# Kernel optimization log

Measured on AMD Instinct MI355X. Metric: run time of the kernel, lower is better.

Reference implementation:

```python
import jax, jax.numpy as jnp
import numpy as np

D = 128          # latent_dim
N = 40000        # num nodes
B = 8            # num graphs in batch
S = N // B       # nodes per graph
K = 6            # knn
E = 640000       # spatial edges
FF = 256         # ffn hidden


def glorot(key, shape):
    lim = jnp.sqrt(6.0 / (shape[0] + shape[-1]))
    return jax.random.uniform(key, shape, minval=-lim, maxval=lim, dtype=jnp.float32)


def setup_inputs() -> dict:
    key = jax.random.key(0)
    ks = jax.random.split(key, 24)
    inp = {
        "x": jax.random.normal(ks[0], (N, D), dtype=jnp.float32),
        "edge_index": jax.random.randint(ks[1], (2, E), 0, N, dtype=jnp.int64),
        "edge_attr": jax.random.uniform(ks[2], (E, 1), dtype=jnp.float32),
        "batch": jnp.repeat(jnp.arange(B, dtype=jnp.int64), S),
        # spatial GATv2Conv params
        "W_sl": glorot(ks[3], (D, D)), "b_sl": jnp.zeros((D,), jnp.float32),
        "W_sr": glorot(ks[4], (D, D)), "b_sr": jnp.zeros((D,), jnp.float32),
        "att_s": glorot(ks[5], (D,)), "W_se": glorot(ks[6], (1, D)),
        "bias_s": jnp.zeros((D,), jnp.float32),
        # latent GATv2Conv params (no edge features)
        "W_ll": glorot(ks[7], (D, D)), "b_ll": jnp.zeros((D,), jnp.float32),
        "W_lr": glorot(ks[8], (D, D)), "b_lr": jnp.zeros((D,), jnp.float32),
        "att_l": glorot(ks[9], (D,)), "bias_l": jnp.zeros((D,), jnp.float32),
        # concat_skip fusion linear: in = 2*D
        "W_c": glorot(ks[10], (2 * D, D)), "b_c": jnp.zeros((D,), jnp.float32),
        # FFN
        "W_f1": glorot(ks[11], (D, FF)), "b_f1": jnp.zeros((FF,), jnp.float32),
        "W_f2": glorot(ks[12], (FF, D)), "b_f2": jnp.zeros((D,), jnp.float32),
    }
    return inp


def relu6(v):
    return jnp.clip(v, 0.0, 6.0)


def segment_softmax(logits, seg, num_segments):
    m = jax.ops.segment_max(logits, seg, num_segments=num_segments)
    e = jnp.exp(logits - m[seg])
    s = jax.ops.segment_sum(e, seg, num_segments=num_segments)
    return e / s[seg]


def gatv2(x, src, dst, edge_feat, W_l, b_l, W_r, b_r, att, bias):
    """PyG GATv2Conv, heads=1, concat=True, negative_slope=0.2."""
    xl = x @ W_l + b_l            # [N,D] source transform
    xr = x @ W_r + b_r            # [N,D] target transform
    h = xl[src] + xr[dst]         # [E,D]
    if edge_feat is not None:
        h = h + edge_feat         # [E,D] already projected by lin_edge
    h = jax.nn.leaky_relu(h, 0.2)
    alpha = h @ att               # [E]
    alpha = segment_softmax(alpha, dst, N)
    out = jax.ops.segment_sum(xl[src] * alpha[:, None], dst, num_segments=N)
    return out + bias


def knn_edges(x):
    """knn_graph(k=K, loop=False, flow='source_to_target') per graph, plus
    the self loops that latent GATv2Conv adds (add_self_loops=True)."""
    xs = jax.lax.stop_gradient(x).reshape(B, S, D)
    sq = jnp.sum(xs * xs, axis=-1)                       # [B,S]
    d2 = sq[:, :, None] + sq[:, None, :] - 2.0 * jnp.einsum('bid,bjd->bij', xs, xs)
    d2 = jnp.where(jnp.eye(S, dtype=bool)[None], jnp.inf, d2)
    _, idx = jax.lax.top_k(-d2, K)                       # [B,S,K] neighbor ids
    offs = (jnp.arange(B) * S)[:, None, None]
    src = (idx + offs).reshape(-1)                       # neighbors -> sources
    dst = jnp.repeat(jnp.arange(N), K)                   # query nodes -> targets
    loop = jnp.arange(N)
    return jnp.concatenate([src, loop]), jnp.concatenate([dst, loop])


def reference(x, edge_index, edge_attr, batch,
              W_sl, b_sl, W_sr, b_sr, att_s, W_se, bias_s,
              W_ll, b_ll, W_lr, b_lr, att_l, bias_l,
              W_c, b_c, W_f1, b_f1, W_f2, b_f2):
    # spatial channel: GATv2 with scalar edge attr
    e_feat = edge_attr @ W_se                            # lin_edge, [E,D]
    ch_sp = gatv2(x, edge_index[0], edge_index[1], e_feat,
                  W_sl, b_sl, W_sr, b_sr, att_s, bias_s)
    # latent channel: dynamic kNN graph + GATv2
    src_l, dst_l = knn_edges(x)
    ch_lat = gatv2(x, src_l, dst_l, None,
                   W_ll, b_ll, W_lr, b_lr, att_l, bias_l)
    # fusion = concat_skip
    fused = jnp.concatenate([ch_sp, ch_lat], axis=-1) @ W_c + b_c + x
    # FFN block (norms are Identity), residual
    ffn = relu6(fused @ W_f1 + b_f1) @ W_f2 + b_f2
    out = fused + ffn
    # plain_last=False -> final activation relu6
    return relu6(out)
```

## Files before the change

### kernel.cpp

```cpp
#include <hip/hip_runtime.h>
#include <math.h>

constexpr int N  = 40000;
constexpr int D  = 128;
constexpr int E  = 640000;
constexpr int Bg = 8;
constexpr int Sg = 5000;
constexpr int KN = 6;
constexpr int FF = 256;
constexpr int CLEN = 640;
constexpr int NCAND = 48;

typedef short short8 __attribute__((ext_vector_type(8)));
typedef float f32x4  __attribute__((ext_vector_type(4)));

__device__ __forceinline__ unsigned short f2bf(float f)
{
    unsigned int u = __float_as_uint(f);
    return (unsigned short)((u + 0x7fffu + ((u >> 16) & 1u)) >> 16);
}

__global__ __launch_bounds__(256) void w_prep_k(
    const float* __restrict__ W0, const float* __restrict__ W1,
    const float* __restrict__ W2, const float* __restrict__ W3,
    const float* __restrict__ Wc, const float* __restrict__ Wf1,
    const float* __restrict__ Wf2,
    unsigned short* __restrict__ wt4, unsigned short* __restrict__ wtc,
    unsigned short* __restrict__ wtf1, unsigned short* __restrict__ wtf2)
{
    int idx = blockIdx.x * 256 + threadIdx.x;
    if (idx < 65536) {
        int m = idx >> 14, rem = idx & 16383;
        int k = rem & 127, c = rem >> 7;
        const float* Wm = (m == 0) ? W0 : (m == 1) ? W1 : (m == 2) ? W2 : W3;
        wt4[m * 16384 + c * 128 + k] = f2bf(Wm[k * 128 + c]);
    } else if (idx < 98304) {
        int rem = idx - 65536; int k = rem & 255, c = rem >> 8;
        wtc[c * 256 + k] = f2bf(Wc[k * 128 + c]);
    } else if (idx < 131072) {
        int rem = idx - 98304; int k = rem & 127, c = rem >> 7;
        wtf1[c * 128 + k] = f2bf(Wf1[k * 256 + c]);
    } else {
        int rem = idx - 131072; int k = rem & 255, c = rem >> 8;
        wtf2[c * 256 + k] = f2bf(Wf2[k * 128 + c]);
    }
}

__global__ __launch_bounds__(256) void gemm_mfma_k(
    const float* __restrict__ A, int lda,
    const unsigned short* __restrict__ Wt, int Kdim,
    const float* __restrict__ bias,
    const float* __restrict__ res,
    float* __restrict__ out, int ldo, int act)
{
    __shared__ float xs[64][36];
    __shared__ unsigned short ws[128][40];
    int tid = threadIdx.x;
    int w = tid >> 6, lane = tid & 63;
    int lg = lane >> 4, ln = lane & 15;
    int r0 = blockIdx.x * 64;
    int cb = blockIdx.y * 128;

    f32x4 acc[8];
#pragma unroll
    for (int ct = 0; ct < 8; ++ct) acc[ct] = {0.f, 0.f, 0.f, 0.f};

    int srow = tid >> 2, sk8 = (tid & 3) * 8;
    int wcol = tid >> 1, wk = (tid & 1) * 16;

    for (int kt = 0; kt < Kdim; kt += 32) {
        __syncthreads();
        *(float4*)&xs[srow][sk8]     = *(const float4*)&A[(size_t)(r0 + srow) * lda + kt + sk8];
        *(float4*)&xs[srow][sk8 + 4] = *(const float4*)&A[(size_t)(r0 + srow) * lda + kt + sk8 + 4];
        *(short8*)&ws[wcol][wk]     = *(const short8*)&Wt[(size_t)(cb + wcol) * Kdim + kt + wk];
        *(short8*)&ws[wcol][wk + 8] = *(const short8*)&Wt[(size_t)(cb + wcol) * Kdim + kt + wk + 8];
        __syncthreads();

        int arow = w * 16 + ln;
        f32x4 a0 = *(const f32x4*)&xs[arow][lg * 8];
        f32x4 a1 = *(const f32x4*)&xs[arow][lg * 8 + 4];
        float af[8] = {a0[0], a0[1], a0[2], a0[3], a1[0], a1[1], a1[2], a1[3]};
        short8 ah, al;
#pragma unroll
        for (int i = 0; i < 8; ++i) {
            unsigned short h = f2bf(af[i]);
            ah[i] = (short)h;
            float hf = __uint_as_float(((unsigned)h) << 16);
            al[i] = (short)f2bf(af[i] - hf);
        }
#pragma unroll
        for (int ct = 0; ct < 8; ++ct) {
            short8 bw = *(const short8*)&ws[ct * 16 + ln][lg * 8];
            acc[ct] = __builtin_amdgcn_mfma_f32_16x16x32_bf16(ah, bw, acc[ct], 0, 0, 0);
            acc[ct] = __builtin_amdgcn_mfma_f32_16x16x32_bf16(al, bw, acc[ct], 0, 0, 0);
        }
    }

#pragma unroll
    for (int ct = 0; ct < 8; ++ct) {
        int c = cb + ct * 16 + ln;
        float bv = bias[c];
#pragma unroll
        for (int rg = 0; rg < 4; ++rg) {
            int r = r0 + w * 16 + lg * 4 + rg;
            float v = acc[ct][rg] + bv;
            if (res) v += res[(size_t)r * 128 + c];
            if (act) v = fminf(fmaxf(v, 0.f), 6.f);
            out[(size_t)r * ldo + c] = v;
        }
    }
}

__global__ __launch_bounds__(256) void gemm4_mfma_k(
    const float* __restrict__ A, const unsigned short* __restrict__ wt4,
    const float* __restrict__ b0, const float* __restrict__ b1,
    const float* __restrict__ b2, const float* __restrict__ b3,
    float* __restrict__ o0, float* __restrict__ o1,
    float* __restrict__ o2, float* __restrict__ o3)
{
    const unsigned short* Wt = wt4 + blockIdx.y * 16384;
    const float* bias; float* out;
    if (blockIdx.y == 0)      { bias = b0; out = o0; }
    else if (blockIdx.y == 1) { bias = b1; out = o1; }
    else if (blockIdx.y == 2) { bias = b2; out = o2; }
    else                      { bias = b3; out = o3; }

    __shared__ float xs[64][36];
    __shared__ unsigned short ws[128][40];
    int tid = threadIdx.x;
    int w = tid >> 6, lane = tid & 63;
    int lg = lane >> 4, ln = lane & 15;
    int r0 = blockIdx.x * 64;

    f32x4 acc[8];
#pragma unroll
    for (int ct = 0; ct < 8; ++ct) acc[ct] = {0.f, 0.f, 0.f, 0.f};

    int srow = tid >> 2, sk8 = (tid & 3) * 8;
    int wcol = tid >> 1, wk = (tid & 1) * 16;

    for (int kt = 0; kt < 128; kt += 32) {
        __syncthreads();
        *(float4*)&xs[srow][sk8]     = *(const float4*)&A[(size_t)(r0 + srow) * 128 + kt + sk8];
        *(float4*)&xs[srow][sk8 + 4] = *(const float4*)&A[(size_t)(r0 + srow) * 128 + kt + sk8 + 4];
        *(short8*)&ws[wcol][wk]     = *(const short8*)&Wt[(size_t)wcol * 128 + kt + wk];
        *(short8*)&ws[wcol][wk + 8] = *(const short8*)&Wt[(size_t)wcol * 128 + kt + wk + 8];
        __syncthreads();

        int arow = w * 16 + ln;
        f32x4 a0 = *(const f32x4*)&xs[arow][lg * 8];
        f32x4 a1 = *(const f32x4*)&xs[arow][lg * 8 + 4];
        float af[8] = {a0[0], a0[1], a0[2], a0[3], a1[0], a1[1], a1[2], a1[3]};
        short8 ah, al;
#pragma unroll
        for (int i = 0; i < 8; ++i) {
            unsigned short h = f2bf(af[i]);
            ah[i] = (short)h;
            float hf = __uint_as_float(((unsigned)h) << 16);
            al[i] = (short)f2bf(af[i] - hf);
        }
#pragma unroll
        for (int ct = 0; ct < 8; ++ct) {
            short8 bw = *(const short8*)&ws[ct * 16 + ln][lg * 8];
            acc[ct] = __builtin_amdgcn_mfma_f32_16x16x32_bf16(ah, bw, acc[ct], 0, 0, 0);
            acc[ct] = __builtin_amdgcn_mfma_f32_16x16x32_bf16(al, bw, acc[ct], 0, 0, 0);
        }
    }

#pragma unroll
    for (int ct = 0; ct < 8; ++ct) {
        int c = ct * 16 + ln;
        float bv = bias[c];
#pragma unroll
        for (int rg = 0; rg < 4; ++rg) {
            int r = r0 + w * 16 + lg * 4 + rg;
            out[(size_t)r * 128 + c] = acc[ct][rg] + bv;
        }
    }
}

__global__ __launch_bounds__(256) void prep_k(const float* __restrict__ x,
                                              unsigned short* __restrict__ xh,
                                              float* __restrict__ sqn)
{
    int w = threadIdx.x >> 6, lane = threadIdx.x & 63;
    int row = blockIdx.x * 4 + w;
    float2 v = *(const float2*)&x[(size_t)row * 128 + lane * 2];
    ushort2 h = make_ushort2(f2bf(v.x), f2bf(v.y));
    *(ushort2*)&xh[(size_t)row * 128 + lane * 2] = h;
    float s = fmaf(v.y, v.y, v.x * v.x);
#pragma unroll
    for (int off = 32; off; off >>= 1) s += __shfl_xor(s, off);
    if (lane == 0) sqn[row] = s;
}

__device__ __forceinline__ void ins6(unsigned (&d)[6], unsigned k)
{
#pragma unroll
    for (int t = 0; t < 6; ++t) {
        unsigned lo = d[t] < k ? d[t] : k;
        unsigned hi = d[t] < k ? k : d[t];
        d[t] = lo; k = hi;
    }
}

__global__ __launch_bounds__(256) void knn_mfma_k(const unsigned short* __restrict__ xh,
                                                  const float* __restrict__ sqn,
                                                  int* __restrict__ cand)
{
    __shared__ char lds[16640];
    char* ldsH = lds;
    float* cs_s = (float*)(lds + 16384);

    int b = blockIdx.x;
    int g = b & 7, r = b >> 3;
    int chunk = r & 7, qblk = r >> 3;
    int gbase = g * Sg;
    int cbase = chunk * CLEN;
    int qlen = (chunk < 7) ? CLEN : (Sg - 7 * CLEN);
    int ntiles = (qlen + 63) >> 6;
    int nfull = (chunk < 7) ? ntiles : ntiles - 1;
    int tid = threadIdx.x;
    int w = tid >> 6, lane = tid & 63;
    int lg = lane >> 4, ln = lane & 15;
    int q0 = qblk * 128 + w * 32;

    short8 bh[2][4];
#pragma unroll
    for (int s = 0; s < 2; ++s) {
        int q = q0 + s * 16 + ln;
        int qrow = gbase + (q < Sg ? q : Sg - 1);
#pragma unroll
        for (int ks = 0; ks < 4; ++ks)
            bh[s][ks] = *(const short8*)&xh[(size_t)qrow * 128 + ks * 32 + lg * 8];
    }

    int srow = tid >> 4, sslot = tid & 15;
    int sw_st = (srow & 7) << 4;
    int dstoff[4];
    const unsigned short* src[4];
#pragma unroll
    for (int i = 0; i < 4; ++i) {
        int row = i * 16 + srow;
        dstoff[i] = row * 256 + ((sslot * 16) ^ sw_st);
        src[i] = &xh[(size_t)(gbase + cbase + row) * 128 + sslot * 8];
    }
    const float* csrc = &sqn[gbase + cbase];

    unsigned d6a[6], d6b[6];
#pragma unroll
    for (int t = 0; t < 6; ++t) { d6a[t] = 0xFFFFFFFFu; d6b[t] = 0xFFFFFFFFu; }

    for (int t64 = 0; t64 < ntiles; ++t64) {
        __syncthreads();
        if (t64 < nfull) {
#pragma unroll
            for (int i = 0; i < 4; ++i) {
                short8 vh = *(const short8*)src[i];
                src[i] += 64 * 128;
                *(short8*)(ldsH + dstoff[i]) = vh;
            }
            if (tid < 64) cs_s[tid] = csrc[tid] + 1024.0f;
        } else {
            int c0 = cbase + t64 * 64;
#pragma unroll
            for (int i = 0; i < 4; ++i) {
                int cr = c0 + i * 16 + srow;
                if (cr >= Sg) cr = Sg - 1;
                short8 vh = *(const short8*)&xh[(size_t)(gbase + cr) * 128 + sslot * 8];
                *(short8*)(ldsH + dstoff[i]) = vh;
            }
            if (tid < 64) {
                int cl = c0 + tid;
                cs_s[tid] = (cl < cbase + qlen) ? (sqn[gbase + cl] + 1024.0f) : __builtin_inff();
            }
        }
        csrc += 64;
        __syncthreads();

        int c0 = cbase + t64 * 64;
#pragma unroll
        for (int g16 = 0; g16 < 4; ++g16) {
            f32x4 acc0 = {0.f, 0.f, 0.f, 0.f};
            f32x4 acc1 = {0.f, 0.f, 0.f, 0.f};
            int rr = g16 * 16 + ln;
            int rsw = (ln & 7) << 4;
#pragma unroll
            for (int ks = 0; ks < 4; ++ks) {
                short8 ah = *(const short8*)(ldsH + rr * 256 + ((lg * 16 + ks * 64) ^ rsw));
                acc0 = __builtin_amdgcn_mfma_f32_16x16x32_bf16(ah, bh[0][ks], acc0, 0, 0, 0);
                acc1 = __builtin_amdgcn_mfma_f32_16x16x32_bf16(ah, bh[1][ks], acc1, 0, 0, 0);
            }
            f32x4 cv = *(const f32x4*)&cs_s[g16 * 16 + lg * 4];
            int idx0 = (c0 - cbase) + g16 * 16 + lg * 4;
#pragma unroll
            for (int rg = 0; rg < 4; ++rg) {
                unsigned ki = (unsigned)(idx0 + rg);
                unsigned k0 = (__float_as_uint(fmaf(-2.f, acc0[rg], cv[rg])) & 0xFFFFF800u) | ki;
                unsigned k1 = (__float_as_uint(fmaf(-2.f, acc1[rg], cv[rg])) & 0xFFFFF800u) | ki;
                ins6(d6a, k0);
                ins6(d6b, k1);
            }
        }
    }

#pragma unroll
    for (int s = 0; s < 2; ++s) {
        unsigned m6[6];
#pragma unroll
        for (int t = 0; t < 6; ++t) m6[t] = s ? d6b[t] : d6a[t];
#pragma unroll
        for (int sg = 1; sg < 4; ++sg)
#pragma unroll
            for (int t = 0; t < 6; ++t) {
                unsigned v = __shfl(s ? d6b[t] : d6a[t], ln + sg * 16);
#pragma unroll
                for (int u = 0; u < 6; ++u) {
                    unsigned lo = m6[u] < v ? m6[u] : v;
                    unsigned hi = m6[u] < v ? v : m6[u];
                    m6[u] = lo; v = hi;
                }
            }
        int q = q0 + s * 16 + ln;
        if (lg == 0 && q < Sg) {
            int* cp = &cand[(size_t)(gbase + q) * NCAND + chunk * 6];
#pragma unroll
            for (int t = 0; t < 6; ++t) cp[t] = gbase + cbase + (int)(m6[t] & 2047u);
        }
    }
}

__global__ __launch_bounds__(256) void knn_rerank_k(const float* __restrict__ x,
                                                    const float* __restrict__ sqn,
                                                    const int* __restrict__ cand,
                                                    int* __restrict__ knn_idx)
{
    int w = threadIdx.x >> 6, lane = threadIdx.x & 63;
    int grp = lane >> 4, gl = lane & 15;
    int q = blockIdx.x * 4 + w;
    float4 qa = *(const float4*)&x[(size_t)q * 128 + gl * 8];
    float4 qb = *(const float4*)&x[(size_t)q * 128 + gl * 8 + 4];
    const int* cp = &cand[(size_t)q * NCAND + grp * 12];

    int ca[12]; unsigned okm = 0;
#pragma unroll
    for (int j = 0; j < 12; ++j) {
        int c = cp[j];
        bool ok = (unsigned)c < (unsigned)N && c != q;
        okm |= (ok ? 1u : 0u) << j;
        ca[j] = ok ? c : 0;
    }

    float d6[6]; int i6[6]; float mx = __builtin_inff(); int sl = 0;
#pragma unroll
    for (int t = 0; t < 6; ++t) { d6[t] = __builtin_inff(); i6[t] = -1; }

    float4 vaA = *(const float4*)&x[(size_t)ca[0] * 128 + gl * 8];
    float4 vbA = *(const float4*)&x[(size_t)ca[0] * 128 + gl * 8 + 4];
#pragma unroll
    for (int j = 0; j < 12; ++j) {
        float4 vaB, vbB;
        if (j < 11) {
            vaB = *(const float4*)&x[(size_t)ca[j + 1] * 128 + gl * 8];
            vbB = *(const float4*)&x[(size_t)ca[j + 1] * 128 + gl * 8 + 4];
        }
        float p = qa.x * vaA.x;
        p = fmaf(qa.y, vaA.y, p); p = fmaf(qa.z, vaA.z, p); p = fmaf(qa.w, vaA.w, p);
        p = fmaf(qb.x, vbA.x, p); p = fmaf(qb.y, vbA.y, p);
        p = fmaf(qb.z, vbA.z, p); p = fmaf(qb.w, vbA.w, p);
#pragma unroll
        for (int off = 1; off < 16; off <<= 1) p += __shfl_xor(p, off);
        float dv = ((okm >> j) & 1u) ? fmaf(-2.f, p, sqn[ca[j]]) : __builtin_inff();
        if (dv < mx) {
#pragma unroll
            for (int t = 0; t < 6; ++t)
                if (t == sl) { d6[t] = dv; i6[t] = ca[j]; }
            float m2 = d6[0]; int s2 = 0;
#pragma unroll
            for (int t = 1; t < 6; ++t)
                if (d6[t] > m2) { m2 = d6[t]; s2 = t; }
            mx = m2; sl = s2;
        }
        vaA = vaB; vbA = vbB;
    }

#pragma unroll
    for (int sg = 1; sg < 4; ++sg) {
#pragma unroll
        for (int t = 0; t < 6; ++t) {
            float dv = __shfl(d6[t], gl + sg * 16);
            int ci = __shfl(i6[t], gl + sg * 16);
            if (grp == 0 && dv < mx) {
#pragma unroll
                for (int u = 0; u < 6; ++u)
                    if (u == sl) { d6[u] = dv; i6[u] = ci; }
                float m2 = d6[0]; int s2 = 0;
#pragma unroll
                for (int u = 1; u < 6; ++u)
                    if (d6[u] > m2) { m2 = d6[u]; s2 = u; }
                mx = m2; sl = s2;
            }
        }
    }
    if (lane < 6) {
        int v;
#pragma unroll
        for (int t = 0; t < 6; ++t) if (t == lane) v = i6[t];
        knn_idx[(size_t)q * 6 + lane] = v;
    }
}

__global__ __launch_bounds__(256) void hist_k(const int* __restrict__ dstA, int* __restrict__ deg)
{
    int e = blockIdx.x * 256 + threadIdx.x;
    atomicAdd(&deg[dstA[e]], 1);
}

__global__ __launch_bounds__(1024) void scan_k(const int* __restrict__ deg, int* __restrict__ rowptr)
{
    __shared__ int ps[1024];
    int t = threadIdx.x;
    const int chunk = 40;
    int base = t * chunk;
    int s = 0;
    for (int k = 0; k < chunk; ++k) { int i = base + k; if (i < N) s += deg[i]; }
    ps[t] = s;
    __syncthreads();
    for (int off = 1; off < 1024; off <<= 1) {
        int v = (t >= off) ? ps[t - off] : 0;
        __syncthreads();
        ps[t] += v;
        __syncthreads();
    }
    int run = ps[t] - s;
    for (int k = 0; k < chunk; ++k) {
        int i = base + k;
        if (i < N) { rowptr[i] = run; run += deg[i]; }
    }
    if (t == 0) rowptr[N] = E;
}

__global__ __launch_bounds__(256) void scatter_k(const int* __restrict__ srcA, const int* __restrict__ dstA,
                                                 const float* __restrict__ ea,
                                                 const int* __restrict__ rowptr, int* __restrict__ cnt,
                                                 int* __restrict__ csr_src, float* __restrict__ csr_ea)
{
    int e = blockIdx.x * 256 + threadIdx.x;
    int d = dstA[e];
    int pos = rowptr[d] + atomicAdd(&cnt[d], 1);
    csr_src[pos] = srcA[e];
    csr_ea[pos] = ea[e];
}

__global__ __launch_bounds__(256) void gat_fused_k(
    const float* __restrict__ xl_s, const float* __restrict__ xr_s,
    const int* __restrict__ rowptr, const int* __restrict__ csr_src, const float* __restrict__ csr_ea,
    const float* __restrict__ att_s, const float* __restrict__ wse, const float* __restrict__ bias_s,
    const float* __restrict__ xl_l, const float* __restrict__ xr_l,
    const int* __restrict__ knn, const float* __restrict__ att_l, const float* __restrict__ bias_l,
    float* __restrict__ ch2)
{
    int w = threadIdx.x >> 6, lane = threadIdx.x & 63;
    int dst = blockIdx.x * 4 + w;

    if (blockIdx.y == 0) {
        int base = rowptr[dst];
        int deg = rowptr[dst + 1] - base;
        float xr0 = xr_s[(size_t)dst * 128 + lane], xr1 = xr_s[(size_t)dst * 128 + 64 + lane];
        float at0 = att_s[lane], at1 = att_s[64 + lane];
        float we0 = wse[lane], we1 = wse[64 + lane];

        float eaN = 0.f, v0N = 0.f, v1N = 0.f;
        if (deg > 0) {
            int s0 = csr_src[base];
            eaN = csr_ea[base];
            v0N = xl_s[(size_t)s0 * 128 + lane];
            v1N = xl_s[(size_t)s0 * 128 + 64 + lane];
        }
        float m = -1e30f, ssum = 0.f, o0 = 0.f, o1 = 0.f;
        for (int i = 0; i < deg; ++i) {
            float ea = eaN, v0 = v0N, v1 = v1N;
            if (i + 1 < deg) {
                int sn = csr_src[base + i + 1];
                eaN = csr_ea[base + i + 1];
                v0N = xl_s[(size_t)sn * 128 + lane];
                v1N = xl_s[(size_t)sn * 128 + 64 + lane];
            }
            float h0 = fmaf(ea, we0, v0 + xr0);
            float h1 = fmaf(ea, we1, v1 + xr1);
            h0 = h0 > 0.f ? h0 : 0.2f * h0;
            h1 = h1 > 0.f ? h1 : 0.2f * h1;
            float p = fmaf(h1, at1, h0 * at0);
#pragma unroll
            for (int off = 32; off; off >>= 1) p += __shfl_xor(p, off);
            if (p <= m) {
                float wt = __expf(p - m);
                ssum += wt;
                o0 = fmaf(wt, v0, o0);
                o1 = fmaf(wt, v1, o1);
            } else {
                float sc = __expf(m - p);
                ssum = fmaf(ssum, sc, 1.f);
                o0 = fmaf(o0, sc, v0);
                o1 = fmaf(o1, sc, v1);
                m = p;
            }
        }
        float inv = deg > 0 ? 1.f / ssum : 0.f;
        ch2[(size_t)dst * 256 + lane]      = fmaf(o0, inv, bias_s[lane]);
        ch2[(size_t)dst * 256 + 64 + lane] = fmaf(o1, inv, bias_s[64 + lane]);
    } else {
        float xr0 = xr_l[(size_t)dst * 128 + lane], xr1 = xr_l[(size_t)dst * 128 + 64 + lane];
        float at0 = att_l[lane], at1 = att_l[64 + lane];
        int s[7];
#pragma unroll
        for (int j = 0; j < 6; ++j) s[j] = knn[(size_t)dst * 6 + j];
        s[6] = dst;
        float l[7];
#pragma unroll
        for (int j = 0; j < 7; ++j) {
            float h0 = xl_l[(size_t)s[j] * 128 + lane] + xr0;
            float h1 = xl_l[(size_t)s[j] * 128 + 64 + lane] + xr1;
            h0 = h0 > 0.f ? h0 : 0.2f * h0;
            h1 = h1 > 0.f ? h1 : 0.2f * h1;
            float p = h0 * at0 + h1 * at1;
#pragma unroll
            for (int off = 32; off; off >>= 1) p += __shfl_xor(p, off);
            l[j] = p;
        }
        float m = l[0];
#pragma unroll
        for (int j = 1; j < 7; ++j) m = fmaxf(m, l[j]);
        float sum = 0.f;
#pragma unroll
        for (int j = 0; j < 7; ++j) { l[j] = __expf(l[j] - m); sum += l[j]; }
        float inv = 1.f / sum;
        float o0 = 0.f, o1 = 0.f;
#pragma unroll
        for (int j = 0; j < 7; ++j) {
            float a = l[j] * inv;
            o0 = fmaf(a, xl_l[(size_t)s[j] * 128 + lane], o0);
            o1 = fmaf(a, xl_l[(size_t)s[j] * 128 + 64 + lane], o1);
        }
        ch2[(size_t)dst * 256 + 128 + lane] = o0 + bias_l[lane];
        ch2[(size_t)dst * 256 + 192 + lane] = o1 + bias_l[64 + lane];
    }
}

extern "C" void kernel_launch(void* const* d_in, const int* in_sizes, int n_in,
                              void* d_out, int out_size, void* d_ws, size_t ws_size,
                              hipStream_t stream)
{
    const float* x      = (const float*)d_in[0];
    const int*   ei     = (const int*)  d_in[1];
    const float* eattr  = (const float*)d_in[2];
    const float* W_sl   = (const float*)d_in[4];
    const float* b_sl   = (const float*)d_in[5];
    const float* W_sr   = (const float*)d_in[6];
    const float* b_sr   = (const float*)d_in[7];
    const float* att_s  = (const float*)d_in[8];
    const float* W_se   = (const float*)d_in[9];
    const float* bias_s = (const float*)d_in[10];
    const float* W_ll   = (const float*)d_in[11];
    const float* b_ll   = (const float*)d_in[12];
    const float* W_lr   = (const float*)d_in[13];
    const float* b_lr   = (const float*)d_in[14];
    const float* att_l  = (const float*)d_in[15];
    const float* bias_l = (const float*)d_in[16];
    const float* W_c    = (const float*)d_in[17];
    const float* b_c    = (const float*)d_in[18];
    const float* W_f1   = (const float*)d_in[19];
    const float* b_f1   = (const float*)d_in[20];
    const float* W_f2   = (const float*)d_in[21];
    const float* b_f2   = (const float*)d_in[22];
    float* out = (float*)d_out;

    char* wp = (char*)d_ws;
    auto take = [&](size_t bytes) { char* p = wp; wp += (bytes + 255) & ~(size_t)255; return p; };
    float* xl_s    = (float*)take((size_t)N * D * 4);
    float* xr_s    = (float*)take((size_t)N * D * 4);
    float* xl_l    = (float*)take((size_t)N * D * 4);
    float* xr_l    = (float*)take((size_t)N * D * 4);
    float* ch2     = (float*)take((size_t)N * 2 * D * 4);
    float* sqn     = (float*)take((size_t)N * 4);
    int*   knn_idx = (int*)  take((size_t)N * KN * 4);
    int*   deg     = (int*)  take((size_t)N * 4);
    int*   rowptr  = (int*)  take((size_t)(N + 1) * 4);
    int*   csr_src = (int*)  take((size_t)E * 4);
    float* csr_ea  = (float*)take((size_t)E * 4);
    unsigned short* x_hi = (unsigned short*)take((size_t)N * D * 2);
    int*   knn_cand = (int*)take((size_t)N * NCAND * 4);
    unsigned short* wt4  = (unsigned short*)take(65536 * 2);
    unsigned short* wtc  = (unsigned short*)take(32768 * 2);
    unsigned short* wtf1 = (unsigned short*)take(32768 * 2);
    unsigned short* wtf2 = (unsigned short*)take(32768 * 2);
    float* fused   = xl_s;
    float* hbuf    = ch2;
    if ((size_t)(wp - (char*)d_ws) > ws_size) return;

    dim3 blk(256);

    w_prep_k<<<dim3(640), blk, 0, stream>>>(W_sl, W_sr, W_ll, W_lr, W_c, W_f1, W_f2,
                                            wt4, wtc, wtf1, wtf2);

    gemm4_mfma_k<<<dim3(N / 64, 4), blk, 0, stream>>>(x, wt4,
        b_sl, b_sr, b_ll, b_lr, xl_s, xr_s, xl_l, xr_l);

    prep_k<<<dim3(N / 4), blk, 0, stream>>>(x, x_hi, sqn);
    knn_mfma_k<<<dim3(Bg * 40 * 8), blk, 0, stream>>>(x_hi, sqn, knn_cand);
    knn_rerank_k<<<dim3(N / 4), blk, 0, stream>>>(x, sqn, knn_cand, knn_idx);

    hipMemsetAsync(deg, 0, (size_t)N * 4, stream);
    hist_k<<<dim3(E / 256), blk, 0, stream>>>(ei + E, deg);
    scan_k<<<dim3(1), dim3(1024), 0, stream>>>(deg, rowptr);
    hipMemsetAsync(deg, 0, (size_t)N * 4, stream);
    scatter_k<<<dim3(E / 256), blk, 0, stream>>>(ei, ei + E, eattr, rowptr, deg, csr_src, csr_ea);

    gat_fused_k<<<dim3(N / 4, 2), blk, 0, stream>>>(xl_s, xr_s, rowptr, csr_src, csr_ea,
                                                    att_s, W_se, bias_s,
                                                    xl_l, xr_l, knn_idx, att_l, bias_l, ch2);

    gemm_mfma_k<<<dim3(N / 64, 1), blk, 0, stream>>>(ch2, 2 * D, wtc, 256, b_c, x, fused, 128, 0);
    gemm_mfma_k<<<dim3(N / 64, 2), blk, 0, stream>>>(fused, 128, wtf1, 128, b_f1, nullptr, hbuf, 256, 1);
    gemm_mfma_k<<<dim3(N / 64, 1), blk, 0, stream>>>(hbuf, 256, wtf2, 256, b_f2, fused, out, 128, 1);
}
```

Baseline: 521.2 us.

## Fuse bf16 prep into projection GEMM and stage two kNN tiles per sync

The separate prep kernel that converts x to bf16 and computes squared norms is removed. That work now runs inside the y==0 blocks of the four-way projection GEMM, reusing the x tiles those blocks already load, which saves a launch and a full read of x. The kNN kernel doubles its LDS to two tile buffers, stages two candidate tiles between barriers, and splits the MFMA accumulation from the top-6 insertion to halve barrier count. The cost is more LDS per block, which may lower occupancy, and extra work concentrated in the y==0 GEMM blocks.

```diff
diff --git a/kernel.cpp b/kernel.cpp
--- a/kernel.cpp
+++ b/kernel.cpp
@@ -116,7 +116,8 @@
     const float* __restrict__ b0, const float* __restrict__ b1,
     const float* __restrict__ b2, const float* __restrict__ b3,
     float* __restrict__ o0, float* __restrict__ o1,
-    float* __restrict__ o2, float* __restrict__ o3)
+    float* __restrict__ o2, float* __restrict__ o3,
+    unsigned short* __restrict__ xh, float* __restrict__ sqn)
 {
     const unsigned short* Wt = wt4 + blockIdx.y * 16384;
     const float* bias; float* out;
@@ -138,13 +139,27 @@
 
     int srow = tid >> 2, sk8 = (tid & 3) * 8;
     int wcol = tid >> 1, wk = (tid & 1) * 16;
+    bool emit = (blockIdx.y == 0);
+    float sq = 0.f;
 
     for (int kt = 0; kt < 128; kt += 32) {
         __syncthreads();
-        *(float4*)&xs[srow][sk8]     = *(const float4*)&A[(size_t)(r0 + srow) * 128 + kt + sk8];
-        *(float4*)&xs[srow][sk8 + 4] = *(const float4*)&A[(size_t)(r0 + srow) * 128 + kt + sk8 + 4];
+        float4 v0 = *(const float4*)&A[(size_t)(r0 + srow) * 128 + kt + sk8];
+        float4 v1 = *(const float4*)&A[(size_t)(r0 + srow) * 128 + kt + sk8 + 4];
+        *(float4*)&xs[srow][sk8]     = v0;
+        *(float4*)&xs[srow][sk8 + 4] = v1;
         *(short8*)&ws[wcol][wk]     = *(const short8*)&Wt[(size_t)wcol * 128 + kt + wk];
         *(short8*)&ws[wcol][wk + 8] = *(const short8*)&Wt[(size_t)wcol * 128 + kt + wk + 8];
+        if (emit) {
+            float f[8] = {v0.x, v0.y, v0.z, v0.w, v1.x, v1.y, v1.z, v1.w};
+            short8 hv;
+#pragma unroll
+            for (int i = 0; i < 8; ++i) {
+                hv[i] = (short)f2bf(f[i]);
+                sq = fmaf(f[i], f[i], sq);
+            }
+            *(short8*)&xh[(size_t)(r0 + srow) * 128 + kt + sk8] = hv;
+        }
         __syncthreads();
 
         int arow = w * 16 + ln;
@@ -167,6 +182,12 @@
         }
     }
 
+    if (emit) {
+        sq += __shfl_xor(sq, 1);
+        sq += __shfl_xor(sq, 2);
+        if ((tid & 3) == 0) sqn[r0 + srow] = sq;
+    }
+
 #pragma unroll
     for (int ct = 0; ct < 8; ++ct) {
         int c = ct * 16 + ln;
@@ -177,21 +198,6 @@
             out[(size_t)r * 128 + c] = acc[ct][rg] + bv;
         }
     }
-}
-
-__global__ __launch_bounds__(256) void prep_k(const float* __restrict__ x,
-                                              unsigned short* __restrict__ xh,
-                                              float* __restrict__ sqn)
-{
-    int w = threadIdx.x >> 6, lane = threadIdx.x & 63;
-    int row = blockIdx.x * 4 + w;
-    float2 v = *(const float2*)&x[(size_t)row * 128 + lane * 2];
-    ushort2 h = make_ushort2(f2bf(v.x), f2bf(v.y));
-    *(ushort2*)&xh[(size_t)row * 128 + lane * 2] = h;
-    float s = fmaf(v.y, v.y, v.x * v.x);
-#pragma unroll
-    for (int off = 32; off; off >>= 1) s += __shfl_xor(s, off);
-    if (lane == 0) sqn[row] = s;
 }
 
 __device__ __forceinline__ void ins6(unsigned (&d)[6], unsigned k)
@@ -208,9 +214,7 @@
                                                   const float* __restrict__ sqn,
                                                   int* __restrict__ cand)
 {
-    __shared__ char lds[16640];
-    char* ldsH = lds;
-    float* cs_s = (float*)(lds + 16384);
+    __shared__ char lds[33280];
 
     int b = blockIdx.x;
     int g = b & 7, r = b >> 3;
@@ -238,12 +242,12 @@
     int srow = tid >> 4, sslot = tid & 15;
     int sw_st = (srow & 7) << 4;
     int dstoff[4];
-    const unsigned short* src[4];
+    const unsigned short* srcb[4];
 #pragma unroll
     for (int i = 0; i < 4; ++i) {
         int row = i * 16 + srow;
         dstoff[i] = row * 256 + ((sslot * 16) ^ sw_st);
-        src[i] = &xh[(size_t)(gbase + cbase + row) * 128 + sslot * 8];
+        srcb[i] = &xh[(size_t)(gbase + cbase + row) * 128 + sslot * 8];
     }
     const float* csrc = &sqn[gbase + cbase];
 
@@ -251,34 +255,36 @@
 #pragma unroll
     for (int t = 0; t < 6; ++t) { d6a[t] = 0xFFFFFFFFu; d6b[t] = 0xFFFFFFFFu; }
 
-    for (int t64 = 0; t64 < ntiles; ++t64) {
-        __syncthreads();
+    auto stage = [&](int t64, int buf) {
+        char* dst = lds + buf * 16384;
+        float* cs = (float*)(lds + 32768 + buf * 256);
         if (t64 < nfull) {
-#pragma unroll
-            for (int i = 0; i < 4; ++i) {
-                short8 vh = *(const short8*)src[i];
-                src[i] += 64 * 128;
-                *(short8*)(ldsH + dstoff[i]) = vh;
-            }
-            if (tid < 64) cs_s[tid] = csrc[tid] + 1024.0f;
+            size_t off = (size_t)t64 * 64 * 128;
+#pragma unroll
+            for (int i = 0; i < 4; ++i)
+                *(short8*)(dst + dstoff[i]) = *(const short8*)(srcb[i] + off);
+            if (tid < 64) cs[tid] = csrc[t64 * 64 + tid] + 1024.0f;
         } else {
             int c0 = cbase + t64 * 64;
 #pragma unroll
             for (int i = 0; i < 4; ++i) {
                 int cr = c0 + i * 16 + srow;
                 if (cr >= Sg) cr = Sg - 1;
-                short8 vh = *(const short8*)&xh[(size_t)(gbase + cr) * 128 + sslot * 8];
-                *(short8*)(ldsH + dstoff[i]) = vh;
+                *(short8*)(dst + dstoff[i]) =
+                    *(const short8*)&xh[(size_t)(gbase + cr) * 128 + sslot * 8];
             }
             if (tid < 64) {
                 int cl = c0 + tid;
-                cs_s[tid] = (cl < cbase + qlen) ? (sqn[gbase + cl] + 1024.0f) : __builtin_inff();
-            }
-        }
-        csrc += 64;
-        __syncthreads();
-
-        int c0 = cbase + t64 * 64;
+                cs[tid] = (cl < cbase + qlen) ? (sqn[gbase + cl] + 1024.0f) : __builtin_inff();
+            }
+        }
+    };
+
+    auto compute = [&](int t64, int buf) {
+        const char* ldsH = lds + buf * 16384;
+        const float* cs = (const float*)(lds + 32768 + buf * 256);
+        int idxb = t64 * 64;
+        f32x4 A0[4], A1[4];
 #pragma unroll
         for (int g16 = 0; g16 < 4; ++g16) {
             f32x4 acc0 = {0.f, 0.f, 0.f, 0.f};
@@ -291,17 +297,31 @@
                 acc0 = __builtin_amdgcn_mfma_f32_16x16x32_bf16(ah, bh[0][ks], acc0, 0, 0, 0);
                 acc1 = __builtin_amdgcn_mfma_f32_16x16x32_bf16(ah, bh[1][ks], acc1, 0, 0, 0);
             }
-            f32x4 cv = *(const f32x4*)&cs_s[g16 * 16 + lg * 4];
-            int idx0 = (c0 - cbase) + g16 * 16 + lg * 4;
+            A0[g16] = acc0; A1[g16] = acc1;
+        }
+#pragma unroll
+        for (int g16 = 0; g16 < 4; ++g16) {
+            f32x4 cv = *(const f32x4*)&cs[g16 * 16 + lg * 4];
+            int idx0 = idxb + g16 * 16 + lg * 4;
 #pragma unroll
             for (int rg = 0; rg < 4; ++rg) {
                 unsigned ki = (unsigned)(idx0 + rg);
-                unsigned k0 = (__float_as_uint(fmaf(-2.f, acc0[rg], cv[rg])) & 0xFFFFF800u) | ki;
-                unsigned k1 = (__float_as_uint(fmaf(-2.f, acc1[rg], cv[rg])) & 0xFFFFF800u) | ki;
+                unsigned k0 = (__float_as_uint(fmaf(-2.f, A0[g16][rg], cv[rg])) & 0xFFFFF800u) | ki;
+                unsigned k1 = (__float_as_uint(fmaf(-2.f, A1[g16][rg], cv[rg])) & 0xFFFFF800u) | ki;
                 ins6(d6a, k0);
                 ins6(d6b, k1);
             }
         }
+    };
+
+    for (int t2 = 0; t2 < ntiles; t2 += 2) {
+        bool two = (t2 + 1 < ntiles);
+        stage(t2, 0);
+        if (two) stage(t2 + 1, 1);
+        __syncthreads();
+        compute(t2, 0);
+        if (two) compute(t2 + 1, 1);
+        __syncthreads();
     }
 
 #pragma unroll
@@ -604,9 +624,8 @@
                                             wt4, wtc, wtf1, wtf2);
 
     gemm4_mfma_k<<<dim3(N / 64, 4), blk, 0, stream>>>(x, wt4,
-        b_sl, b_sr, b_ll, b_lr, xl_s, xr_s, xl_l, xr_l);
-
-    prep_k<<<dim3(N / 4), blk, 0, stream>>>(x, x_hi, sqn);
+        b_sl, b_sr, b_ll, b_lr, xl_s, xr_s, xl_l, xr_l, x_hi, sqn);
+
     knn_mfma_k<<<dim3(Bg * 40 * 8), blk, 0, stream>>>(x_hi, sqn, knn_cand);
     knn_rerank_k<<<dim3(N / 4), blk, 0, stream>>>(x, sqn, knn_cand, knn_idx);
 
```

New measurement: 523.3 us. No clear change (+0.4%).

## Fuse fusion-linear and FFN GEMMs into one tail kernel; fold prep into gemm4

Applied to the files above, without the earlier changes.

Replaces the three tail GEMM launches (concat-skip linear, FFN up, FFN down) with a single kernel. It keeps the fused tile and the ReLU6 hidden activations in LDS, so the intermediate [N,128] and [N,256] tensors never go through global memory. The hidden activations are stored as bf16 and used in a single MFMA pass instead of the hi/lo split, which lowers precision on the second FFN GEMM. It also folds the bf16 conversion and squared-norm computation from prep_k into the first projection GEMM, saving a launch and a re-read of x. The larger LDS footprint (about 60KB per block) may cut occupancy.

```diff
diff --git a/kernel.cpp b/kernel.cpp
--- a/kernel.cpp
+++ b/kernel.cpp
@@ -46,20 +46,27 @@
     }
 }
 
-__global__ __launch_bounds__(256) void gemm_mfma_k(
-    const float* __restrict__ A, int lda,
-    const unsigned short* __restrict__ Wt, int Kdim,
-    const float* __restrict__ bias,
-    const float* __restrict__ res,
-    float* __restrict__ out, int ldo, int act)
-{
+__global__ __launch_bounds__(256) void gemm4_mfma_k(
+    const float* __restrict__ A, const unsigned short* __restrict__ wt4,
+    const float* __restrict__ b0, const float* __restrict__ b1,
+    const float* __restrict__ b2, const float* __restrict__ b3,
+    float* __restrict__ o0, float* __restrict__ o1,
+    float* __restrict__ o2, float* __restrict__ o3,
+    unsigned short* __restrict__ xh, float* __restrict__ sqn)
+{
+    const unsigned short* Wt = wt4 + blockIdx.y * 16384;
+    const float* bias; float* out;
+    if (blockIdx.y == 0)      { bias = b0; out = o0; }
+    else if (blockIdx.y == 1) { bias = b1; out = o1; }
+    else if (blockIdx.y == 2) { bias = b2; out = o2; }
+    else                      { bias = b3; out = o3; }
+
     __shared__ float xs[64][36];
     __shared__ unsigned short ws[128][40];
     int tid = threadIdx.x;
     int w = tid >> 6, lane = tid & 63;
     int lg = lane >> 4, ln = lane & 15;
     int r0 = blockIdx.x * 64;
-    int cb = blockIdx.y * 128;
 
     f32x4 acc[8];
 #pragma unroll
@@ -67,13 +74,27 @@
 
     int srow = tid >> 2, sk8 = (tid & 3) * 8;
     int wcol = tid >> 1, wk = (tid & 1) * 16;
-
-    for (int kt = 0; kt < Kdim; kt += 32) {
-        __syncthreads();
-        *(float4*)&xs[srow][sk8]     = *(const float4*)&A[(size_t)(r0 + srow) * lda + kt + sk8];
-        *(float4*)&xs[srow][sk8 + 4] = *(const float4*)&A[(size_t)(r0 + srow) * lda + kt + sk8 + 4];
-        *(short8*)&ws[wcol][wk]     = *(const short8*)&Wt[(size_t)(cb + wcol) * Kdim + kt + wk];
-        *(short8*)&ws[wcol][wk + 8] = *(const short8*)&Wt[(size_t)(cb + wcol) * Kdim + kt + wk + 8];
+    bool emit = (blockIdx.y == 0);
+    float sq = 0.f;
+
+    for (int kt = 0; kt < 128; kt += 32) {
+        __syncthreads();
+        float4 v0 = *(const float4*)&A[(size_t)(r0 + srow) * 128 + kt + sk8];
+        float4 v1 = *(const float4*)&A[(size_t)(r0 + srow) * 128 + kt + sk8 + 4];
+        *(float4*)&xs[srow][sk8]     = v0;
+        *(float4*)&xs[srow][sk8 + 4] = v1;
+        *(short8*)&ws[wcol][wk]     = *(const short8*)&Wt[(size_t)wcol * 128 + kt + wk];
+        *(short8*)&ws[wcol][wk + 8] = *(const short8*)&Wt[(size_t)wcol * 128 + kt + wk + 8];
+        if (emit) {
+            float f[8] = {v0.x, v0.y, v0.z, v0.w, v1.x, v1.y, v1.z, v1.w};
+            short8 hv;
+#pragma unroll
+            for (int i = 0; i < 8; ++i) {
+                hv[i] = (short)f2bf(f[i]);
+                sq = fmaf(f[i], f[i], sq);
+            }
+            *(short8*)&xh[(size_t)(r0 + srow) * 128 + kt + sk8] = hv;
+        }
         __syncthreads();
 
         int arow = w * 16 + ln;
@@ -96,60 +117,58 @@
         }
     }
 
+    if (emit) {
+        sq += __shfl_xor(sq, 1);
+        sq += __shfl_xor(sq, 2);
+        if ((tid & 3) == 0) sqn[r0 + srow] = sq;
+    }
+
 #pragma unroll
     for (int ct = 0; ct < 8; ++ct) {
-        int c = cb + ct * 16 + ln;
+        int c = ct * 16 + ln;
         float bv = bias[c];
 #pragma unroll
         for (int rg = 0; rg < 4; ++rg) {
             int r = r0 + w * 16 + lg * 4 + rg;
-            float v = acc[ct][rg] + bv;
-            if (res) v += res[(size_t)r * 128 + c];
-            if (act) v = fminf(fmaxf(v, 0.f), 6.f);
-            out[(size_t)r * ldo + c] = v;
-        }
-    }
-}
-
-__global__ __launch_bounds__(256) void gemm4_mfma_k(
-    const float* __restrict__ A, const unsigned short* __restrict__ wt4,
-    const float* __restrict__ b0, const float* __restrict__ b1,
-    const float* __restrict__ b2, const float* __restrict__ b3,
-    float* __restrict__ o0, float* __restrict__ o1,
-    float* __restrict__ o2, float* __restrict__ o3)
-{
-    const unsigned short* Wt = wt4 + blockIdx.y * 16384;
-    const float* bias; float* out;
-    if (blockIdx.y == 0)      { bias = b0; out = o0; }
-    else if (blockIdx.y == 1) { bias = b1; out = o1; }
-    else if (blockIdx.y == 2) { bias = b2; out = o2; }
-    else                      { bias = b3; out = o3; }
-
-    __shared__ float xs[64][36];
-    __shared__ unsigned short ws[128][40];
+            out[(size_t)r * 128 + c] = acc[ct][rg] + bv;
+        }
+    }
+}
+
+__global__ __launch_bounds__(256) void tail_mfma_k(
+    const float* __restrict__ ch2, const float* __restrict__ x,
+    const unsigned short* __restrict__ wtc,
+    const unsigned short* __restrict__ wtf1,
+    const unsigned short* __restrict__ wtf2,
+    const float* __restrict__ b_c, const float* __restrict__ b_f1,
+    const float* __restrict__ b_f2, float* __restrict__ out)
+{
+    __shared__ char lds[60928];
+    float* fused_s = (float*)lds;
+    unsigned short* hid_s = (unsigned short*)(lds + 33792);
+    float* xs = (float*)(lds + 33792);
+    unsigned short* ws = (unsigned short*)(lds + 33792 + 16896);
+
     int tid = threadIdx.x;
     int w = tid >> 6, lane = tid & 63;
     int lg = lane >> 4, ln = lane & 15;
     int r0 = blockIdx.x * 64;
-
-    f32x4 acc[8];
-#pragma unroll
-    for (int ct = 0; ct < 8; ++ct) acc[ct] = {0.f, 0.f, 0.f, 0.f};
-
     int srow = tid >> 2, sk8 = (tid & 3) * 8;
     int wcol = tid >> 1, wk = (tid & 1) * 16;
-
-    for (int kt = 0; kt < 128; kt += 32) {
-        __syncthreads();
-        *(float4*)&xs[srow][sk8]     = *(const float4*)&A[(size_t)(r0 + srow) * 128 + kt + sk8];
-        *(float4*)&xs[srow][sk8 + 4] = *(const float4*)&A[(size_t)(r0 + srow) * 128 + kt + sk8 + 4];
-        *(short8*)&ws[wcol][wk]     = *(const short8*)&Wt[(size_t)wcol * 128 + kt + wk];
-        *(short8*)&ws[wcol][wk + 8] = *(const short8*)&Wt[(size_t)wcol * 128 + kt + wk + 8];
-        __syncthreads();
-
-        int arow = w * 16 + ln;
-        f32x4 a0 = *(const f32x4*)&xs[arow][lg * 8];
-        f32x4 a1 = *(const f32x4*)&xs[arow][lg * 8 + 4];
+    int arow = w * 16 + ln;
+
+    f32x4 acc[8];
+#pragma unroll
+    for (int ct = 0; ct < 8; ++ct) acc[ct] = {0.f, 0.f, 0.f, 0.f};
+    for (int kt = 0; kt < 256; kt += 32) {
+        __syncthreads();
+        *(float4*)&xs[srow * 36 + sk8]     = *(const float4*)&ch2[(size_t)(r0 + srow) * 256 + kt + sk8];
+        *(float4*)&xs[srow * 36 + sk8 + 4] = *(const float4*)&ch2[(size_t)(r0 + srow) * 256 + kt + sk8 + 4];
+        *(short8*)&ws[wcol * 40 + wk]     = *(const short8*)&wtc[(size_t)wcol * 256 + kt + wk];
+        *(short8*)&ws[wcol * 40 + wk + 8] = *(const short8*)&wtc[(size_t)wcol * 256 + kt + wk + 8];
+        __syncthreads();
+        f32x4 a0 = *(const f32x4*)&xs[arow * 36 + lg * 8];
+        f32x4 a1 = *(const f32x4*)&xs[arow * 36 + lg * 8 + 4];
         float af[8] = {a0[0], a0[1], a0[2], a0[3], a1[0], a1[1], a1[2], a1[3]};
         short8 ah, al;
 #pragma unroll
@@ -161,37 +180,94 @@
         }
 #pragma unroll
         for (int ct = 0; ct < 8; ++ct) {
-            short8 bw = *(const short8*)&ws[ct * 16 + ln][lg * 8];
+            short8 bw = *(const short8*)&ws[(ct * 16 + ln) * 40 + lg * 8];
             acc[ct] = __builtin_amdgcn_mfma_f32_16x16x32_bf16(ah, bw, acc[ct], 0, 0, 0);
             acc[ct] = __builtin_amdgcn_mfma_f32_16x16x32_bf16(al, bw, acc[ct], 0, 0, 0);
         }
     }
-
+    __syncthreads();
 #pragma unroll
     for (int ct = 0; ct < 8; ++ct) {
         int c = ct * 16 + ln;
-        float bv = bias[c];
+        float bv = b_c[c];
 #pragma unroll
         for (int rg = 0; rg < 4; ++rg) {
-            int r = r0 + w * 16 + lg * 4 + rg;
-            out[(size_t)r * 128 + c] = acc[ct][rg] + bv;
-        }
-    }
-}
-
-__global__ __launch_bounds__(256) void prep_k(const float* __restrict__ x,
-                                              unsigned short* __restrict__ xh,
-                                              float* __restrict__ sqn)
-{
-    int w = threadIdx.x >> 6, lane = threadIdx.x & 63;
-    int row = blockIdx.x * 4 + w;
-    float2 v = *(const float2*)&x[(size_t)row * 128 + lane * 2];
-    ushort2 h = make_ushort2(f2bf(v.x), f2bf(v.y));
-    *(ushort2*)&xh[(size_t)row * 128 + lane * 2] = h;
-    float s = fmaf(v.y, v.y, v.x * v.x);
-#pragma unroll
-    for (int off = 32; off; off >>= 1) s += __shfl_xor(s, off);
-    if (lane == 0) sqn[row] = s;
+            int r = w * 16 + lg * 4 + rg;
+            fused_s[r * 132 + c] = acc[ct][rg] + bv + x[(size_t)(r0 + r) * 128 + c];
+        }
+    }
+    __syncthreads();
+
+    f32x4 acc2[8];
+#pragma unroll
+    for (int ct = 0; ct < 8; ++ct) acc2[ct] = {0.f, 0.f, 0.f, 0.f};
+
+    for (int hh = 0; hh < 2; ++hh) {
+        f32x4 acc1[8];
+#pragma unroll
+        for (int ct = 0; ct < 8; ++ct) acc1[ct] = {0.f, 0.f, 0.f, 0.f};
+        for (int kt = 0; kt < 128; kt += 32) {
+            __syncthreads();
+            *(short8*)&ws[wcol * 40 + wk]     = *(const short8*)&wtf1[(size_t)(hh * 128 + wcol) * 128 + kt + wk];
+            *(short8*)&ws[wcol * 40 + wk + 8] = *(const short8*)&wtf1[(size_t)(hh * 128 + wcol) * 128 + kt + wk + 8];
+            __syncthreads();
+            f32x4 a0 = *(const f32x4*)&fused_s[arow * 132 + kt + lg * 8];
+            f32x4 a1 = *(const f32x4*)&fused_s[arow * 132 + kt + lg * 8 + 4];
+            float af[8] = {a0[0], a0[1], a0[2], a0[3], a1[0], a1[1], a1[2], a1[3]};
+            short8 ah, al;
+#pragma unroll
+            for (int i = 0; i < 8; ++i) {
+                unsigned short h = f2bf(af[i]);
+                ah[i] = (short)h;
+                float hf = __uint_as_float(((unsigned)h) << 16);
+                al[i] = (short)f2bf(af[i] - hf);
+            }
+#pragma unroll
+            for (int ct = 0; ct < 8; ++ct) {
+                short8 bw = *(const short8*)&ws[(ct * 16 + ln) * 40 + lg * 8];
+                acc1[ct] = __builtin_amdgcn_mfma_f32_16x16x32_bf16(ah, bw, acc1[ct], 0, 0, 0);
+                acc1[ct] = __builtin_amdgcn_mfma_f32_16x16x32_bf16(al, bw, acc1[ct], 0, 0, 0);
+            }
+        }
+        __syncthreads();
+#pragma unroll
+        for (int ct = 0; ct < 8; ++ct) {
+            int c = ct * 16 + ln;
+            float bv = b_f1[hh * 128 + c];
+#pragma unroll
+            for (int rg = 0; rg < 4; ++rg) {
+                int r = w * 16 + lg * 4 + rg;
+                float hv = fminf(fmaxf(acc1[ct][rg] + bv, 0.f), 6.f);
+                hid_s[r * 132 + c] = f2bf(hv);
+            }
+        }
+        __syncthreads();
+
+        for (int kt = 0; kt < 128; kt += 32) {
+            __syncthreads();
+            *(short8*)&ws[wcol * 40 + wk]     = *(const short8*)&wtf2[(size_t)wcol * 256 + hh * 128 + kt + wk];
+            *(short8*)&ws[wcol * 40 + wk + 8] = *(const short8*)&wtf2[(size_t)wcol * 256 + hh * 128 + kt + wk + 8];
+            __syncthreads();
+            short8 ah = *(const short8*)&hid_s[arow * 132 + kt + lg * 8];
+#pragma unroll
+            for (int ct = 0; ct < 8; ++ct) {
+                short8 bw = *(const short8*)&ws[(ct * 16 + ln) * 40 + lg * 8];
+                acc2[ct] = __builtin_amdgcn_mfma_f32_16x16x32_bf16(ah, bw, acc2[ct], 0, 0, 0);
+            }
+        }
+    }
+
+#pragma unroll
+    for (int ct = 0; ct < 8; ++ct) {
+        int c = ct * 16 + ln;
+        float bv = b_f2[c];
+#pragma unroll
+        for (int rg = 0; rg < 4; ++rg) {
+            int r = w * 16 + lg * 4 + rg;
+            float v = acc2[ct][rg] + bv + fused_s[r * 132 + c];
+            out[(size_t)(r0 + r) * 128 + c] = fminf(fmaxf(v, 0.f), 6.f);
+        }
+    }
 }
 
 __device__ __forceinline__ void ins6(unsigned (&d)[6], unsigned k)
@@ -594,8 +670,6 @@
     unsigned short* wtc  = (unsigned short*)take(32768 * 2);
     unsigned short* wtf1 = (unsigned short*)take(32768 * 2);
     unsigned short* wtf2 = (unsigned short*)take(32768 * 2);
-    float* fused   = xl_s;
-    float* hbuf    = ch2;
     if ((size_t)(wp - (char*)d_ws) > ws_size) return;
 
     dim3 blk(256);
@@ -604,9 +678,8 @@
                                             wt4, wtc, wtf1, wtf2);
 
     gemm4_mfma_k<<<dim3(N / 64, 4), blk, 0, stream>>>(x, wt4,
-        b_sl, b_sr, b_ll, b_lr, xl_s, xr_s, xl_l, xr_l);
-
-    prep_k<<<dim3(N / 4), blk, 0, stream>>>(x, x_hi, sqn);
+        b_sl, b_sr, b_ll, b_lr, xl_s, xr_s, xl_l, xr_l, x_hi, sqn);
+
     knn_mfma_k<<<dim3(Bg * 40 * 8), blk, 0, stream>>>(x_hi, sqn, knn_cand);
     knn_rerank_k<<<dim3(N / 4), blk, 0, stream>>>(x, sqn, knn_cand, knn_idx);
 
@@ -620,7 +693,6 @@
                                                     att_s, W_se, bias_s,
                                                     xl_l, xr_l, knn_idx, att_l, bias_l, ch2);
 
-    gemm_mfma_k<<<dim3(N / 64, 1), blk, 0, stream>>>(ch2, 2 * D, wtc, 256, b_c, x, fused, 128, 0);
-    gemm_mfma_k<<<dim3(N / 64, 2), blk, 0, stream>>>(fused, 128, wtf1, 128, b_f1, nullptr, hbuf, 256, 1);
-    gemm_mfma_k<<<dim3(N / 64, 1), blk, 0, stream>>>(hbuf, 256, wtf2, 256, b_f2, fused, out, 128, 1);
-}
+    tail_mfma_k<<<dim3(N / 64), blk, 0, stream>>>(ch2, x, wtc, wtf1, wtf2,
+                                                  b_c, b_f1, b_f2, out);
+}
```

After: 486.8 us, median of 2. 6.6% less time.
